# Kernel tuning notes

Hardware: AMD Instinct MI355X
Metric: run time of the kernel (lower is better)

Reference implementation:

```python
import jax, jax.numpy as jnp
import numpy as np

B = 256
NUM_ROUTES = 32 * 6 * 6  # 1152
NUM_CAPS = 10
OUT_CH = 16
IN_CH = 8


def squash(x, axis=-1):
    sq = jnp.sum(x * x, axis=axis, keepdims=True)
    return sq * x / ((1.0 + sq) * jnp.sqrt(sq))


def conv2d(x, w, b, stride):
    y = jax.lax.conv_general_dilated(
        x, w, window_strides=(stride, stride), padding='VALID',
        dimension_numbers=('NCHW', 'OIHW', 'NCHW'))
    return y + b[None, :, None, None]


def setup_inputs() -> dict:
    key = jax.random.key(0)
    ks = jax.random.split(key, 12)
    data = jax.random.normal(ks[0], (B, 1, 28, 28), dtype=jnp.float32)
    conv1_w = jax.random.normal(ks[1], (256, 1, 9, 9), dtype=jnp.float32) * 0.1
    conv1_b = jax.random.normal(ks[2], (256,), dtype=jnp.float32) * 0.01
    # 8 primary-capsule convs, each 256->32, k9 s2 (stacked)
    pc_w = jax.random.normal(ks[3], (8, 32, 256, 9, 9), dtype=jnp.float32) * 0.02
    pc_b = jax.random.normal(ks[4], (8, 32), dtype=jnp.float32) * 0.01
    # DigitCaps routing weights (torch.randn init)
    W_dc = jax.random.normal(ks[5], (NUM_ROUTES, NUM_CAPS, OUT_CH, IN_CH), dtype=jnp.float32)
    dec_w1 = jax.random.normal(ks[6], (160, 512), dtype=jnp.float32) * 0.05
    dec_b1 = jnp.zeros((512,), dtype=jnp.float32)
    dec_w2 = jax.random.normal(ks[7], (512, 1024), dtype=jnp.float32) * 0.05
    dec_b2 = jnp.zeros((1024,), dtype=jnp.float32)
    dec_w3 = jax.random.normal(ks[8], (1024, 784), dtype=jnp.float32) * 0.05
    dec_b3 = jnp.zeros((784,), dtype=jnp.float32)
    return dict(data=data, conv1_w=conv1_w, conv1_b=conv1_b, pc_w=pc_w, pc_b=pc_b,
                W_dc=W_dc, dec_w1=dec_w1, dec_b1=dec_b1, dec_w2=dec_w2,
                dec_b2=dec_b2, dec_w3=dec_w3, dec_b3=dec_b3)


def capsnet_forward(data, conv1_w, conv1_b, pc_w, pc_b, W_dc,
                    dec_w1, dec_b1, dec_w2, dec_b2, dec_w3, dec_b3):
    bsz = data.shape[0]
    # ConvLayer: [B,1,28,28] -> [B,256,20,20]
    x = jax.nn.relu(conv2d(data, conv1_w, conv1_b, 1))
    # PrimaryCaps: 8 independent convs fused into one 256-out conv then split
    # [B,256,6,6] viewed as [B,8,32,6,6] matches torch.stack(u, dim=1)
    u = conv2d(x, pc_w.reshape(256, 256, 9, 9), pc_b.reshape(256), 2)
    u = u.reshape(bsz, NUM_ROUTES, IN_CH)  # [B,1152,8]
    u = squash(u)
    # DigitCaps: u_hat[b,r,c,o] = sum_i W[r,c,o,i] * u[b,r,i]
    u_hat = jnp.einsum('rcoi,bri->brco', W_dc, u)  # [B,1152,10,16]
    b_ij = jnp.zeros((NUM_ROUTES, NUM_CAPS), dtype=u_hat.dtype)
    num_iterations = 3
    v = None
    for it in range(num_iterations):
        c_ij = jax.nn.softmax(b_ij, axis=0)            # softmax over routes
        s_j = jnp.einsum('rc,brco->bco', c_ij, u_hat)  # [B,10,16]
        v = squash(s_j, axis=-1)
        if it < num_iterations - 1:
            a_ij = jnp.einsum('brco,bco->rc', u_hat, v) / bsz  # mean over batch
            b_ij = b_ij + a_ij
    output = v[..., None]  # [B,10,16,1]
    # Decoder
    classes = jnp.sqrt(jnp.sum(output ** 2, axis=2))   # [B,10,1]
    classes = jax.nn.softmax(classes, axis=0)          # softmax over batch (as in source)
    idx = jnp.argmax(classes, axis=1)[:, 0]            # [B]
    masked = jnp.eye(NUM_CAPS, dtype=output.dtype)[idx]  # [B,10]
    t = (output * masked[:, :, None, None]).reshape(bsz, -1)  # [B,160]
    h = jax.nn.relu(t @ dec_w1 + dec_b1)
    h = jax.nn.relu(h @ dec_w2 + dec_b2)
    recon = jax.nn.sigmoid(h @ dec_w3 + dec_b3).reshape(bsz, 1, 28, 28)
    return output, recon, masked


def reference(data, conv1_w, conv1_b, pc_w, pc_b, W_dc,
              dec_w1, dec_b1, dec_w2, dec_b2, dec_w3, dec_b3):
    return capsnet_forward(data, conv1_w, conv1_b, pc_w, pc_b, W_dc,
                           dec_w1, dec_b1, dec_w2, dec_b2, dec_w3, dec_b3)
```

## Files before the change

### kernel.cpp

```cpp
#include <hip/hip_runtime.h>
#include <math.h>


typedef __attribute__((ext_vector_type(8))) short short8;
typedef __attribute__((ext_vector_type(4))) float f32x4;

__device__ __forceinline__ unsigned short f2bf(float x) {
  unsigned int u = __float_as_uint(x);
  unsigned int r = (u + 0x7fffu + ((u >> 16) & 1u)) >> 16;
  return (unsigned short)r;
}
__device__ __forceinline__ float bf2f(unsigned short h) {
  return __uint_as_float(((unsigned int)h) << 16);
}
__device__ __forceinline__ void gload16(const void* g, void* l) {
  __builtin_amdgcn_global_load_lds(
      (const __attribute__((address_space(1))) unsigned int*)g,
      (__attribute__((address_space(3))) unsigned int*)l, 16, 0, 0);
}
__device__ __forceinline__ float dot8(const float* w, float4 a, float4 b) {
  return w[0]*a.x + w[1]*a.y + w[2]*a.z + w[3]*a.w +
         w[4]*b.x + w[5]*b.y + w[6]*b.z + w[7]*b.w;
}

__global__ void w1prep(const float* __restrict__ w1,
                       unsigned short* __restrict__ w1th,
                       unsigned short* __restrict__ w1tl)
{
  const int k  = blockIdx.x;
  const int co = threadIdx.x;
  float x = (k < 81) ? w1[co * 81 + k] : 0.f;
  unsigned short h = f2bf(x);
  w1th[co * 96 + k] = h;
  w1tl[co * 96 + k] = f2bf(x - bf2f(h));
}

__global__ __launch_bounds__(256) void conv1_mfma(
    const float* __restrict__ data, const unsigned short* __restrict__ w1th,
    const unsigned short* __restrict__ w1tl, const float* __restrict__ b1,
    unsigned short* __restrict__ xh, unsigned short* __restrict__ xl)
{
  __shared__ float img[1344];
  __shared__ int offt[96];
  const int t   = threadIdx.x;
  const int b   = blockIdx.x >> 1;
  const int coh = blockIdx.x & 1;
  const int lane = t & 63, w = t >> 6;
  const int l15 = lane & 15, l4 = lane >> 4;

  for (int i = t; i < 1344; i += 256) img[i] = (i < 784) ? data[b * 784 + i] : 0.f;
  if (t < 96) offt[t] = (t < 81) ? ((t / 9) * 28 + (t % 9)) : 784;
  __syncthreads();

  short8 bh[3][2], bl[3][2];
  #pragma unroll
  for (int ks = 0; ks < 3; ks++)
    #pragma unroll
    for (int nf = 0; nf < 2; nf++) {
      const int co = coh * 128 + w * 32 + nf * 16 + l15;
      bh[ks][nf] = *(const short8*)(w1th + co * 96 + ks * 32 + l4 * 8);
      bl[ks][nf] = *(const short8*)(w1tl + co * 96 + ks * 32 + l4 * 8);
    }
  int koff[3][8];
  #pragma unroll
  for (int ks = 0; ks < 3; ks++)
    #pragma unroll
    for (int j = 0; j < 8; j++)
      koff[ks][j] = offt[ks * 32 + l4 * 8 + j];
  float bv[2];
  bv[0] = b1[coh * 128 + w * 32 + l15];
  bv[1] = b1[coh * 128 + w * 32 + 16 + l15];

  #pragma unroll 1
  for (int mf = 0; mf < 25; mf++) {
    const int p  = mf * 16 + l15;
    const int oy = p / 20, ox = p - oy * 20;
    const int base = oy * 28 + ox;
    f32x4 acc[2];
    acc[0] = (f32x4){0.f, 0.f, 0.f, 0.f};
    acc[1] = (f32x4){0.f, 0.f, 0.f, 0.f};
    #pragma unroll
    for (int ks = 0; ks < 3; ks++) {
      short8 ah, al;
      #pragma unroll
      for (int j = 0; j < 8; j++) {
        float a = img[base + koff[ks][j]];
        unsigned short h = f2bf(a);
        ah[j] = (short)h;
        al[j] = (short)f2bf(a - bf2f(h));
      }
      #pragma unroll
      for (int nf = 0; nf < 2; nf++) {
        f32x4 a4 = acc[nf];
        a4 = __builtin_amdgcn_mfma_f32_16x16x32_bf16(ah, bh[ks][nf], a4, 0, 0, 0);
        a4 = __builtin_amdgcn_mfma_f32_16x16x32_bf16(al, bh[ks][nf], a4, 0, 0, 0);
        a4 = __builtin_amdgcn_mfma_f32_16x16x32_bf16(ah, bl[ks][nf], a4, 0, 0, 0);
        acc[nf] = a4;
      }
    }
    #pragma unroll
    for (int nf = 0; nf < 2; nf++) {
      const int co = coh * 128 + w * 32 + nf * 16 + l15;
      #pragma unroll
      for (int reg = 0; reg < 4; reg++) {
        const int p2 = mf * 16 + l4 * 4 + reg;
        float v = fmaxf(acc[nf][reg] + bv[nf], 0.f);
        unsigned short h = f2bf(v);
        const int pix = b * 400 + p2;
        xh[pix * 256 + co] = h;
        xl[pix * 256 + co] = f2bf(v - bf2f(h));
      }
    }
  }
}

__global__ void wprep(const float* __restrict__ pw, unsigned short* __restrict__ wh,
                      unsigned short* __restrict__ wl)
{
  const int co = blockIdx.x;
  const int t  = threadIdx.x;
  __shared__ float slab[20736];
  for (int i = t; i < 20736; i += 256) slab[i] = pw[co * 20736 + i];
  __syncthreads();
  const int cc = t >> 5, ci5 = t & 31;
  for (int k = 0; k < 81; k++) {
    float x = slab[t * 81 + k];
    unsigned short h = f2bf(x);
    int dst = ((k * 8 + cc) * 256 + co) * 32 + ci5;
    wh[dst] = h;
    wl[dst] = f2bf(x - bf2f(h));
  }
}

__global__ __launch_bounds__(256) void conv2_mfma(
    const unsigned short* __restrict__ xh, const unsigned short* __restrict__ xl,
    const unsigned short* __restrict__ wh, const unsigned short* __restrict__ wl,
    float* __restrict__ part)
{
  __shared__ char lds[49152];
  const int t   = threadIdx.x;
  const int blk = blockIdx.x;
  const int mt  = blk % 144;
  const int kg  = blk / 144;
  const int m0  = mt * 64;
  const int lane = t & 63;
  const int w    = t >> 6;
  const int l15  = lane & 15, l4 = lane >> 4;

  const int g0  = t ^ ((t >> 3) & 7);
  const int ar0 = g0 >> 3;
  const int ach = g0 & 7;
  auto pixbase = [&](int pix) {
    int ab = pix / 36; int sp = pix - ab * 36;
    int oy = sp / 6;   int ox = sp - oy * 6;
    return ((ab * 20 + 2 * oy) * 20 + 2 * ox) * 256;
  };
  const int abase0 = pixbase(m0 + ar0) + ach * 8;
  const int abase1 = pixbase(m0 + ar0 + 32) + ach * 8;

  const int bofs = (w * 64 + l15) * 32 + l4 * 8;

  f32x4 acc[4][4];
  #pragma unroll
  for (int i = 0; i < 4; i++)
    #pragma unroll
    for (int j = 0; j < 4; j++) acc[i][j] = (f32x4){0.f, 0.f, 0.f, 0.f};

  const int ky0 = kg * 3;

  auto stageA = [&](int buf, int xy, int ci0) {
    char* base = lds + buf * 16384;
    gload16(xh + abase0 + xy + ci0, base + t * 16);
    gload16(xh + abase1 + xy + ci0, base + 4096  + t * 16);
    gload16(xl + abase0 + xy + ci0, base + 8192  + t * 16);
    gload16(xl + abase1 + xy + ci0, base + 12288 + t * 16);
  };

  stageA(0, ky0 * 20 * 256, 0);
  int kyc = ky0, kxc = 0, cc2 = 0;
  #pragma unroll 1
  for (int s = 0; s < 108; ++s) {
    const int kkc = (kyc * 9 + kxc) * 8 + cc2 * 2;
    short8 b_h[4][2], b_l[4][2];
    #pragma unroll
    for (int ks = 0; ks < 2; ks++) {
      const unsigned short* bhp = wh + (kkc + ks) * 8192 + bofs;
      const unsigned short* blp = wl + (kkc + ks) * 8192 + bofs;
      #pragma unroll
      for (int nf = 0; nf < 4; nf++) {
        b_h[nf][ks] = *(const short8*)(bhp + nf * 512);
        b_l[nf][ks] = *(const short8*)(blp + nf * 512);
      }
    }
    cc2++; if (cc2 == 4) { cc2 = 0; kxc++; if (kxc == 9) { kxc = 0; kyc++; } }
    if (s < 107) {
      stageA((s + 1) % 3, (kyc * 20 + kxc) * 256, cc2 * 64);
      asm volatile("s_waitcnt vmcnt(20)" ::: "memory");
    } else {
      asm volatile("s_waitcnt vmcnt(16)" ::: "memory");
    }
    asm volatile("s_barrier" ::: "memory");

    char* base = lds + (s % 3) * 16384;
    #pragma unroll
    for (int ks = 0; ks < 2; ks++) {
      short8 a_h[4], a_l[4];
      #pragma unroll
      for (int mf = 0; mf < 4; mf++) {
        const int row = mf * 16 + l15;
        const int off = ((row * 8 + ks * 4 + l4) ^ (l15 & 7)) << 4;
        a_h[mf] = *(const short8*)(base + off);
        a_l[mf] = *(const short8*)(base + 8192 + off);
      }
      __builtin_amdgcn_s_setprio(1);
      #pragma unroll
      for (int nf = 0; nf < 4; nf++)
        #pragma unroll
        for (int mf = 0; mf < 4; mf++) {
          f32x4 a = acc[mf][nf];
          a = __builtin_amdgcn_mfma_f32_16x16x32_bf16(a_h[mf], b_h[nf][ks], a, 0, 0, 0);
          a = __builtin_amdgcn_mfma_f32_16x16x32_bf16(a_l[mf], b_h[nf][ks], a, 0, 0, 0);
          a = __builtin_amdgcn_mfma_f32_16x16x32_bf16(a_h[mf], b_l[nf][ks], a, 0, 0, 0);
          acc[mf][nf] = a;
        }
      __builtin_amdgcn_s_setprio(0);
    }
  }

  float* pout = part + kg * 2359296;
  #pragma unroll
  for (int mf = 0; mf < 4; mf++)
    #pragma unroll
    for (int nf = 0; nf < 4; nf++) {
      const int co = w * 64 + nf * 16 + l15;
      #pragma unroll
      for (int reg = 0; reg < 4; reg++) {
        const int pix = m0 + mf * 16 + l4 * 4 + reg;
        const int b  = pix / 36;
        const int sp = pix - b * 36;
        pout[b * 9216 + co * 36 + sp] = acc[mf][nf][reg];
      }
    }
}

__global__ void combine_squash(const float* __restrict__ part,
                               const float* __restrict__ pb,
                               float* __restrict__ uT)
{
  const int id = blockIdx.x * 256 + threadIdx.x;
  const int b = id / 1152;
  const int r = id % 1152;
  const float* p0 = part + b * 9216 + r * 8;
  float v[8];
  #pragma unroll
  for (int i = 0; i < 8; i++) v[i] = p0[i] + p0[2359296 + i] + p0[4718592 + i];
  #pragma unroll
  for (int i = 0; i < 8; i++) v[i] += pb[(r * 8 + i) / 36];
  float sq = 0.f;
  #pragma unroll
  for (int i = 0; i < 8; i++) sq += v[i] * v[i];
  float scale = sq / ((1.f + sq) * sqrtf(sq));
  #pragma unroll
  for (int i = 0; i < 8; i++) uT[(r * 256 + b) * 8 + i] = v[i] * scale;
}

__global__ __launch_bounds__(256) void s_pass(
    const float* __restrict__ uT, const float* __restrict__ Wdc,
    const float* __restrict__ bij, float* __restrict__ spart, int uniform)
{
  const int c  = blockIdx.x % 10;
  const int q  = blockIdx.x / 10;
  const int r0 = q * 18;
  const int t  = threadIdx.x;
  __shared__ float wsm[18 * 128];
  __shared__ float cw[18];
  __shared__ float red[8];

  #pragma unroll
  for (int k = 0; k < 9; k++) {
    int idx = t + k * 256;
    int r = idx >> 7, i = idx & 127;
    wsm[idx] = Wdc[((r0 + r) * 10 + c) * 128 + i];
  }
  if (uniform) {
    if (t < 18) cw[t] = 1.f / 1152.f;
  } else {
    float bv[5]; float m = -1e30f;
    #pragma unroll
    for (int rr = 0; rr < 5; rr++) {
      int r = t + rr * 256;
      bv[rr] = (r < 1152) ? bij[c * 1152 + r] : -1e30f;
      m = fmaxf(m, bv[rr]);
    }
    #pragma unroll
    for (int off = 32; off; off >>= 1) m = fmaxf(m, __shfl_down(m, off, 64));
    if ((t & 63) == 0) red[t >> 6] = m;
    __syncthreads();
    m = fmaxf(fmaxf(red[0], red[1]), fmaxf(red[2], red[3]));
    float ssum = 0.f;
    #pragma unroll
    for (int rr = 0; rr < 5; rr++)
      ssum += (t + rr * 256 < 1152) ? expf(bv[rr] - m) : 0.f;
    #pragma unroll
    for (int off = 32; off; off >>= 1) ssum += __shfl_down(ssum, off, 64);
    if ((t & 63) == 0) red[4 + (t >> 6)] = ssum;
    __syncthreads();
    float inv = 1.f / (red[4] + red[5] + red[6] + red[7]);
    if (t < 18) cw[t] = expf(bij[c * 1152 + r0 + t] - m) * inv;
  }
  __syncthreads();

  const float4* up = (const float4*)(uT + (r0 * 256 + t) * 8);
  float acc[16];
  #pragma unroll
  for (int o = 0; o < 16; o++) acc[o] = 0.f;
  #pragma unroll 1
  for (int r = 0; r < 18; r++) {
    float4 x0 = up[r * 512], x1 = up[r * 512 + 1];
    float cwr = cw[r];
    const float* wr = &wsm[r * 128];
    #pragma unroll
    for (int o = 0; o < 16; o++) {
      const float4 wa = *(const float4*)(wr + o * 8);
      const float4 wb = *(const float4*)(wr + o * 8 + 4);
      acc[o] += cwr * (wa.x*x0.x + wa.y*x0.y + wa.z*x0.z + wa.w*x0.w
                     + wb.x*x1.x + wb.y*x1.y + wb.z*x1.z + wb.w*x1.w);
    }
  }
  float* op = spart + q * 40960 + (t * 10 + c) * 16;
  #pragma unroll
  for (int o = 0; o < 16; o++) op[o] = acc[o];
}

template <int FINAL>
__global__ void reduce_squash(const float* __restrict__ spart, float* __restrict__ outb)
{
  const int id = blockIdx.x * 256 + threadIdx.x;
  float a = 0.f;
  #pragma unroll 8
  for (int q = 0; q < 64; q++) a += spart[q * 40960 + id];
  if (FINAL) { outb[id] = a; return; }
  float sq = a * a;
  #pragma unroll
  for (int off = 8; off; off >>= 1) sq += __shfl_xor(sq, off, 16);
  float scale = sq / ((1.f + sq) * sqrtf(sq));
  const int bc = id >> 4, o = id & 15;
  const int b = bc / 10, c = bc - b * 10;
  outb[(c * 256 + b) * 16 + o] = a * scale;
}

__global__ __launch_bounds__(256) void a_pass(
    const float* __restrict__ uT, const float* __restrict__ W,
    const float* __restrict__ vT, float* __restrict__ bij, int assign)
{
  const int r = blockIdx.x;
  const int t = threadIdx.x;
  __shared__ float wsl[1280];
  __shared__ float lred[4][10];
  for (int i = t; i < 1280; i += 256) wsl[i] = W[r * 1280 + i];
  __syncthreads();
  const float4* up = (const float4*)(uT + (r * 256 + t) * 8);
  float4 ua = up[0], ub = up[1];
  const int lane = t & 63, wid = t >> 6;
  #pragma unroll 1
  for (int c = 0; c < 10; c++) {
    const float* wc = &wsl[c * 128];
    const float4* vp = (const float4*)(vT + (c * 256 + t) * 16);
    float p = 0.f;
    #pragma unroll
    for (int q = 0; q < 4; q++) {
      float4 vq = vp[q];
      p += dot8(wc + (q * 4 + 0) * 8, ua, ub) * vq.x;
      p += dot8(wc + (q * 4 + 1) * 8, ua, ub) * vq.y;
      p += dot8(wc + (q * 4 + 2) * 8, ua, ub) * vq.z;
      p += dot8(wc + (q * 4 + 3) * 8, ua, ub) * vq.w;
    }
    for (int off = 32; off; off >>= 1) p += __shfl_down(p, off, 64);
    if (lane == 0) lred[wid][c] = p;
  }
  __syncthreads();
  if (t < 10) {
    float a = (lred[0][t] + lred[1][t] + lred[2][t] + lred[3][t]) * (1.f / 256.f);
    float o = assign ? 0.f : bij[t * 1152 + r];
    bij[t * 1152 + r] = o + a;
  }
}

__global__ __launch_bounds__(256) void finalize(
    const float* __restrict__ sbuf, float* __restrict__ outp,
    float* __restrict__ maskedo, float* __restrict__ tbuf)
{
  const int b = threadIdx.x;
  __shared__ float nsm[256][10];
  __shared__ float red[8];
  #pragma unroll 1
  for (int c = 0; c < 10; c++) {
    const float4* sp = (const float4*)(sbuf + (b * 10 + c) * 16);
    float4 q0 = sp[0], q1 = sp[1], q2 = sp[2], q3 = sp[3];
    float sq = q0.x*q0.x+q0.y*q0.y+q0.z*q0.z+q0.w*q0.w
             + q1.x*q1.x+q1.y*q1.y+q1.z*q1.z+q1.w*q1.w
             + q2.x*q2.x+q2.y*q2.y+q2.z*q2.z+q2.w*q2.w
             + q3.x*q3.x+q3.y*q3.y+q3.z*q3.z+q3.w*q3.w;
    float scale = sq / ((1.f + sq) * sqrtf(sq));
    float4* op = (float4*)(outp + (b * 10 + c) * 16);
    op[0] = make_float4(q0.x*scale, q0.y*scale, q0.z*scale, q0.w*scale);
    op[1] = make_float4(q1.x*scale, q1.y*scale, q1.z*scale, q1.w*scale);
    op[2] = make_float4(q2.x*scale, q2.y*scale, q2.z*scale, q2.w*scale);
    op[3] = make_float4(q3.x*scale, q3.y*scale, q3.z*scale, q3.w*scale);
    nsm[b][c] = sq / (1.f + sq);
  }
  __syncthreads();
  float sc[10];
  #pragma unroll
  for (int c = 0; c < 10; c++) {
    float x = nsm[b][c];
    float m = x;
    #pragma unroll
    for (int off = 32; off; off >>= 1) m = fmaxf(m, __shfl_down(m, off, 64));
    if ((b & 63) == 0) red[b >> 6] = m;
    __syncthreads();
    m = fmaxf(fmaxf(red[0], red[1]), fmaxf(red[2], red[3]));
    float e = expf(x - m), ss = e;
    #pragma unroll
    for (int off = 32; off; off >>= 1) ss += __shfl_down(ss, off, 64);
    if ((b & 63) == 0) red[4 + (b >> 6)] = ss;
    __syncthreads();
    sc[c] = e / (red[4] + red[5] + red[6] + red[7]);
    __syncthreads();
  }
  int idx = 0; float best = sc[0];
  #pragma unroll
  for (int c = 1; c < 10; c++) if (sc[c] > best) { best = sc[c]; idx = c; }
  #pragma unroll
  for (int c = 0; c < 10; c++) {
    float msk = (c == idx) ? 1.f : 0.f;
    maskedo[b * 10 + c] = msk;
    const float4* op = (const float4*)(outp + (b * 10 + c) * 16);
    float4* tp = (float4*)(tbuf + b * 160 + c * 16);
    #pragma unroll
    for (int qq = 0; qq < 4; qq++) {
      float4 vv = op[qq];
      tp[qq] = make_float4(vv.x * msk, vv.y * msk, vv.z * msk, vv.w * msk);
    }
  }
}

template <int ACT>
__global__ __launch_bounds__(256) void gemm_act(
    const float* __restrict__ A, const float* __restrict__ B,
    const float* __restrict__ bias, float* __restrict__ C, int M, int N, int K)
{
  __shared__ float As[64][17];
  __shared__ float Bs[16][64];
  const int t = threadIdx.x;
  const int tx = t & 15, ty = t >> 4;
  const int m0 = blockIdx.y * 64, n0 = blockIdx.x * 64;
  float acc[4][4] = {};
  for (int kb = 0; kb < K; kb += 16) {
    {
      int row = t >> 2, c4 = (t & 3) * 4;
      float4 av = *(const float4*)(A + (m0 + row) * K + kb + c4);
      As[row][c4+0]=av.x; As[row][c4+1]=av.y; As[row][c4+2]=av.z; As[row][c4+3]=av.w;
    }
    {
      int row = t >> 4, c4 = (t & 15) * 4;
      float4 bv = make_float4(0.f, 0.f, 0.f, 0.f);
      if (n0 + c4 < N) bv = *(const float4*)(B + (kb + row) * N + n0 + c4);
      Bs[row][c4+0]=bv.x; Bs[row][c4+1]=bv.y; Bs[row][c4+2]=bv.z; Bs[row][c4+3]=bv.w;
    }
    __syncthreads();
    #pragma unroll
    for (int kk = 0; kk < 16; kk++) {
      float a_[4], b_[4];
      #pragma unroll
      for (int i = 0; i < 4; i++) a_[i] = As[ty * 4 + i][kk];
      #pragma unroll
      for (int j = 0; j < 4; j++) b_[j] = Bs[kk][tx * 4 + j];
      #pragma unroll
      for (int i = 0; i < 4; i++)
        for (int j = 0; j < 4; j++)
          acc[i][j] = fmaf(a_[i], b_[j], acc[i][j]);
    }
    __syncthreads();
  }
  #pragma unroll
  for (int i = 0; i < 4; i++) {
    int row = m0 + ty * 4 + i;
    #pragma unroll
    for (int j = 0; j < 4; j++) {
      int col = n0 + tx * 4 + j;
      if (col < N) {
        float val = acc[i][j] + bias[col];
        if (ACT == 0) val = val > 0.f ? val : 0.f;
        else          val = 1.f / (1.f + expf(-val));
        C[row * N + col] = val;
      }
    }
  }
}

extern "C" void kernel_launch(void* const* d_in, const int* in_sizes, int n_in,
                              void* d_out, int out_size, void* d_ws, size_t ws_size,
                              hipStream_t stream)
{
  const float* data = (const float*)d_in[0];
  const float* w1   = (const float*)d_in[1];
  const float* b1   = (const float*)d_in[2];
  const float* pw   = (const float*)d_in[3];
  const float* pb   = (const float*)d_in[4];
  const float* Wdc  = (const float*)d_in[5];
  const float* dw1  = (const float*)d_in[6];
  const float* db1  = (const float*)d_in[7];
  const float* dw2  = (const float*)d_in[8];
  const float* db2  = (const float*)d_in[9];
  const float* dw3  = (const float*)d_in[10];
  const float* db3  = (const float*)d_in[11];

  float* out     = (float*)d_out;
  float* outp    = out;
  float* recon   = out + 40960;
  float* maskedo = out + 241664;

  char* wsb = (char*)d_ws;
  unsigned short* x1h = (unsigned short*)(wsb);
  unsigned short* x1l = (unsigned short*)(wsb + 52428800);
  unsigned short* wbh = (unsigned short*)(wsb + 104857600);
  unsigned short* wbl = (unsigned short*)(wsb + 115474432);
  float*  part = (float*)(wsb + 126091264);
  unsigned short* w1th = (unsigned short*)(wsb + 154402816);
  unsigned short* w1tl = (unsigned short*)(wsb + 154451968);
  float* uT   = (float*)(wsb);
  float* vT   = (float*)(wsb + 9437184);
  float* bij  = (float*)(wsb + 9601024);
  float* sbuf = (float*)(wsb + 9647104);
  float* spart= (float*)(wsb + 9810944);
  float* tbuf = (float*)(wsb + 20296704);
  float* h1   = (float*)(wsb + 20460544);
  float* h2   = (float*)(wsb + 20984832);

  w1prep<<<96, 256, 0, stream>>>(w1, w1th, w1tl);
  conv1_mfma<<<512, 256, 0, stream>>>(data, w1th, w1tl, b1, x1h, x1l);
  wprep<<<256, 256, 0, stream>>>(pw, wbh, wbl);
  conv2_mfma<<<432, 256, 0, stream>>>(x1h, x1l, wbh, wbl, part);
  combine_squash<<<1152, 256, 0, stream>>>(part, pb, uT);

  s_pass<<<640, 256, 0, stream>>>(uT, Wdc, bij, spart, 1);
  reduce_squash<0><<<160, 256, 0, stream>>>(spart, vT);
  a_pass<<<1152, 256, 0, stream>>>(uT, Wdc, vT, bij, 1);
  s_pass<<<640, 256, 0, stream>>>(uT, Wdc, bij, spart, 0);
  reduce_squash<0><<<160, 256, 0, stream>>>(spart, vT);
  a_pass<<<1152, 256, 0, stream>>>(uT, Wdc, vT, bij, 0);
  s_pass<<<640, 256, 0, stream>>>(uT, Wdc, bij, spart, 0);
  reduce_squash<1><<<160, 256, 0, stream>>>(spart, sbuf);
  finalize<<<1, 256, 0, stream>>>(sbuf, outp, maskedo, tbuf);

  gemm_act<0><<<dim3(8, 4),  256, 0, stream>>>(tbuf, dw1, db1, h1,    256, 512,  160);
  gemm_act<0><<<dim3(16, 4), 256, 0, stream>>>(h1,   dw2, db2, h2,    256, 1024, 512);
  gemm_act<1><<<dim3(13, 4), 256, 0, stream>>>(h2,   dw3, db3, recon, 256, 784,  1024);
}
```

Measured before the change: 649.1 us.

## Split conv2 K dimension eightfold across input-channel groups for more blocks

Adds a conv2 MFMA variant that splits the reduction over 8 input-channel groups instead of 3, launching 1152 blocks rather than 432 with a smaller triple-buffered LDS tile. combine_squash now sums a variable number of partial buffers. The point is to fill more CUs on the MI355X, at the cost of more partial-sum writes and reads in the combine step. The new path is only taken when the workspace is large enough for 8 partial buffers, otherwise the old kernel runs.

```diff
diff --git a/kernel.cpp b/kernel.cpp
--- a/kernel.cpp
+++ b/kernel.cpp
@@ -132,6 +132,104 @@
   }
 }
 
+__global__ __launch_bounds__(256) void conv2_mfma8(
+    const unsigned short* __restrict__ xh, const unsigned short* __restrict__ xl,
+    const unsigned short* __restrict__ wh, const unsigned short* __restrict__ wl,
+    float* __restrict__ part)
+{
+  __shared__ char lds[24576];
+  const int t   = threadIdx.x;
+  const int blk = blockIdx.x;
+  const int cig = blk & 7;
+  const int mt  = blk >> 3;
+  const int m0  = mt * 64;
+  const int lane = t & 63;
+  const int w    = t >> 6;
+  const int l15  = lane & 15, l4 = lane >> 4;
+
+  const int g0  = t ^ ((t >> 3) & 7);
+  const int ar  = g0 >> 2;
+  const int ach = g0 & 3;
+  auto pixbase = [&](int pix) {
+    int ab = pix / 36; int sp = pix - ab * 36;
+    int oy = sp / 6;   int ox = sp - oy * 6;
+    return ((ab * 20 + 2 * oy) * 20 + 2 * ox) * 256;
+  };
+  const int abase = pixbase(m0 + ar) + cig * 32 + ach * 8;
+
+  const int bofs = (w * 64 + l15) * 32 + l4 * 8;
+
+  f32x4 acc[4][4];
+  #pragma unroll
+  for (int i = 0; i < 4; i++)
+    #pragma unroll
+    for (int j = 0; j < 4; j++) acc[i][j] = (f32x4){0.f, 0.f, 0.f, 0.f};
+
+  auto stageA = [&](int buf, int xy) {
+    char* base = lds + buf * 8192;
+    gload16(xh + abase + xy, base + t * 16);
+    gload16(xl + abase + xy, base + 4096 + t * 16);
+  };
+
+  stageA(0, 0);
+  #pragma unroll 1
+  for (int s = 0; s < 81; ++s) {
+    const int slab = (s * 8 + cig) * 8192 + bofs;
+    short8 b_h[4], b_l[4];
+    #pragma unroll
+    for (int nf = 0; nf < 4; nf++) {
+      b_h[nf] = *(const short8*)(wh + slab + nf * 512);
+      b_l[nf] = *(const short8*)(wl + slab + nf * 512);
+    }
+    if (s < 80) {
+      const int ns = s + 1;
+      const int ky = ns / 9, kx = ns - ky * 9;
+      stageA(ns % 3, (ky * 20 + kx) * 256);
+      asm volatile("s_waitcnt vmcnt(10)" ::: "memory");
+    } else {
+      asm volatile("s_waitcnt vmcnt(8)" ::: "memory");
+    }
+    asm volatile("s_barrier" ::: "memory");
+
+    char* base = lds + (s % 3) * 8192;
+    short8 a_h[4], a_l[4];
+    #pragma unroll
+    for (int mf = 0; mf < 4; mf++) {
+      const int g = (mf * 16 + l15) * 4 + l4;
+      const int off = (g ^ ((g >> 3) & 7)) << 4;
+      a_h[mf] = *(const short8*)(base + off);
+      a_l[mf] = *(const short8*)(base + 4096 + off);
+    }
+    __builtin_amdgcn_s_setprio(1);
+    #pragma unroll
+    for (int nf = 0; nf < 4; nf++)
+      #pragma unroll
+      for (int mf = 0; mf < 4; mf++) {
+        f32x4 a = acc[mf][nf];
+        a = __builtin_amdgcn_mfma_f32_16x16x32_bf16(a_h[mf], b_h[nf], a, 0, 0, 0);
+        a = __builtin_amdgcn_mfma_f32_16x16x32_bf16(a_l[mf], b_h[nf], a, 0, 0, 0);
+        a = __builtin_amdgcn_mfma_f32_16x16x32_bf16(a_h[mf], b_l[nf], a, 0, 0, 0);
+        acc[mf][nf] = a;
+      }
+    __builtin_amdgcn_s_setprio(0);
+  }
+
+  float* pout = part + cig * 2359296;
+  #pragma unroll
+  for (int mf = 0; mf < 4; mf++)
+    #pragma unroll
+    for (int nf = 0; nf < 4; nf++) {
+      const int co = w * 64 + nf * 16 + l15;
+      #pragma unroll
+      for (int reg = 0; reg < 4; reg++) {
+        const int pix = m0 + mf * 16 + l4 * 4 + reg;
+        const int b  = pix / 36;
+        const int sp = pix - b * 36;
+        pout[b * 9216 + co * 36 + sp] = acc[mf][nf][reg];
+      }
+    }
+}
+
 __global__ __launch_bounds__(256) void conv2_mfma(
     const unsigned short* __restrict__ xh, const unsigned short* __restrict__ xl,
     const unsigned short* __restrict__ wh, const unsigned short* __restrict__ wl,
@@ -245,7 +343,7 @@
 
 __global__ void combine_squash(const float* __restrict__ part,
                                const float* __restrict__ pb,
-                               float* __restrict__ uT)
+                               float* __restrict__ uT, int np)
 {
   const int id = blockIdx.x * 256 + threadIdx.x;
   const int b = id / 1152;
@@ -253,7 +351,11 @@
   const float* p0 = part + b * 9216 + r * 8;
   float v[8];
   #pragma unroll
-  for (int i = 0; i < 8; i++) v[i] = p0[i] + p0[2359296 + i] + p0[4718592 + i];
+  for (int i = 0; i < 8; i++) v[i] = p0[i];
+  #pragma unroll 1
+  for (int p = 1; p < np; p++)
+    #pragma unroll
+    for (int i = 0; i < 8; i++) v[i] += p0[p * 2359296 + i];
   #pragma unroll
   for (int i = 0; i < 8; i++) v[i] += pb[(r * 8 + i) / 36];
   float sq = 0.f;
@@ -527,8 +629,13 @@
   unsigned short* wbh = (unsigned short*)(wsb + 104857600);
   unsigned short* wbl = (unsigned short*)(wsb + 115474432);
   float*  part = (float*)(wsb + 126091264);
-  unsigned short* w1th = (unsigned short*)(wsb + 154402816);
-  unsigned short* w1tl = (unsigned short*)(wsb + 154451968);
+  unsigned short* w1th = (unsigned short*)(wsb + 126066688 - 196608);
+  const size_t need8 = 126091264ull + 8ull * 9437184ull + 196608ull;
+  const int use8 = (ws_size >= need8);
+  const size_t w1off = use8 ? (126091264ull + 8ull * 9437184ull)
+                            : (126091264ull + 3ull * 9437184ull);
+  w1th = (unsigned short*)(wsb + w1off);
+  unsigned short* w1tl = (unsigned short*)(wsb + w1off + 98304);
   float* uT   = (float*)(wsb);
   float* vT   = (float*)(wsb + 9437184);
   float* bij  = (float*)(wsb + 9601024);
@@ -541,8 +648,13 @@
   w1prep<<<96, 256, 0, stream>>>(w1, w1th, w1tl);
   conv1_mfma<<<512, 256, 0, stream>>>(data, w1th, w1tl, b1, x1h, x1l);
   wprep<<<256, 256, 0, stream>>>(pw, wbh, wbl);
-  conv2_mfma<<<432, 256, 0, stream>>>(x1h, x1l, wbh, wbl, part);
-  combine_squash<<<1152, 256, 0, stream>>>(part, pb, uT);
+  if (use8) {
+    conv2_mfma8<<<1152, 256, 0, stream>>>(x1h, x1l, wbh, wbl, part);
+    combine_squash<<<1152, 256, 0, stream>>>(part, pb, uT, 8);
+  } else {
+    conv2_mfma<<<432, 256, 0, stream>>>(x1h, x1l, wbh, wbl, part);
+    combine_squash<<<1152, 256, 0, stream>>>(part, pb, uT, 3);
+  }
 
   s_pass<<<640, 256, 0, stream>>>(uT, Wdc, bij, spart, 1);
   reduce_squash<0><<<160, 256, 0, stream>>>(spart, vT);
```

Result: slower. 680.0 us (+4.8%).
